# Performance work log

Measured on AMD Instinct MI355X. Metric: run time of the kernel, lower is better.

## Reference

```python
import jax, jax.numpy as jnp
import numpy as np

IN_DIMS = 32
HID = 64
N_HIDDEN = 5  # tcnn n_hidden_layers = hidden_layers + 1 = 5
OUT_DIMS = 3
BATCH = 2097152


def setup_inputs() -> dict:
    key = jax.random.key(0)
    ks = jax.random.split(key, N_HIDDEN + 2)
    x = jax.random.normal(ks[0], (BATCH, IN_DIMS), dtype=jnp.float32)
    # tcnn FullyFusedMLP has no biases; Kaiming-ish init scale
    W0 = jax.random.normal(ks[1], (IN_DIMS, HID), dtype=jnp.float32) * (1.0 / np.sqrt(IN_DIMS))
    Wh = jax.random.normal(ks[2], (N_HIDDEN - 1, HID, HID), dtype=jnp.float32) * (1.0 / np.sqrt(HID))
    Wo = jax.random.normal(ks[3], (HID, OUT_DIMS), dtype=jnp.float32) * (1.0 / np.sqrt(HID))
    return {"x": x, "W0": W0, "Wh": Wh, "Wo": Wo}


def reference(x, W0, Wh, Wo):
    # input layer -> ReLU
    h = jax.nn.relu(x @ W0)  # [B, 64]
    # 4 more hidden layers of 64->64 with ReLU (small fixed count, unrolled)
    for i in range(Wh.shape[0]):
        h = jax.nn.relu(h @ Wh[i])
    # linear output layer (output_activation = None)
    return h @ Wo  # [B, 3]
```

## Files before the change

kernel.cpp:

```cpp
#include <hip/hip_runtime.h>


typedef __attribute__((ext_vector_type(8))) short short8;
typedef __attribute__((ext_vector_type(4))) float f32x4;

#define BATCH   2097152
#define NBLOCKS 1024
#define NWAVES  (NBLOCKS * 4)
#define ITERS   (BATCH / (NWAVES * 16))
static_assert(BATCH == (size_t)NWAVES * 16 * ITERS, "");

__device__ __forceinline__ unsigned cvt_pk(float a, float b) {
    unsigned r;
    asm("v_cvt_pk_bf16_f32 %0, %1, %2" : "=v"(r) : "v"(a), "v"(b));
    return r;
}

__global__ __launch_bounds__(256, 4)
void mlp_fused(const float* __restrict__ x, const float* __restrict__ W0,
               const float* __restrict__ Wh, const float* __restrict__ Wo,
               float* __restrict__ out)
{
    __shared__ short8 wlds[38][64];

    const int tid  = threadIdx.x;
    const int w    = tid >> 6;
    const int lane = tid & 63;
    const int n = lane & 15;
    const int q = lane >> 4;

    const int gw = blockIdx.x * 4 + w;

    f32x4 raw0, raw1;
    {
        const f32x4* p = (const f32x4*)(x + ((size_t)gw * 16 + n) * 32) + 2 * q;
        raw0 = p[0]; raw1 = p[1];
    }

    int phi[4];
    #pragma unroll
    for (int t = 0; t < 4; ++t)
        phi[t] = 32 * (t >> 1) + 8 * (n >> 2) + 4 * (t & 1) + (n & 3);

    auto build = [&](const float* p) -> short8 {
        union { unsigned u[4]; short8 s; } f;
        #pragma unroll
        for (int i = 0; i < 4; ++i)
            f.u[i] = cvt_pk(p[(2 * i) * 64], p[(2 * i + 1) * 64]);
        return f.s;
    };
    if (w == 0) {
        #pragma unroll
        for (int t = 0; t < 4; ++t)
            wlds[t][lane] = build(W0 + (8 * q) * 64 + phi[t]);
        #pragma unroll
        for (int t = 0; t < 4; ++t)
            #pragma unroll
            for (int c = 0; c < 2; ++c)
                wlds[28 + 2 * t + c][lane] =
                    build(Wh + 3 * 4096 + (32 * c + 8 * q) * 64 + phi[t]);
        #pragma unroll
        for (int c = 0; c < 2; ++c) {
            union { unsigned u[4]; short8 s; } f;
            #pragma unroll
            for (int i = 0; i < 4; ++i) {
                float a = (n < 3) ? Wo[(32 * c + 8 * q + 2 * i)     * 3 + n] : 0.f;
                float b = (n < 3) ? Wo[(32 * c + 8 * q + 2 * i + 1) * 3 + n] : 0.f;
                f.u[i] = cvt_pk(a, b);
            }
            wlds[36 + c][lane] = f.s;
        }
    } else {
        const int l = w - 1;
        #pragma unroll
        for (int t = 0; t < 4; ++t)
            #pragma unroll
            for (int c = 0; c < 2; ++c)
                wlds[4 + 8 * l + 2 * t + c][lane] =
                    build(Wh + l * 4096 + (32 * c + 8 * q) * 64 + phi[t]);
    }
    __syncthreads();

    const f32x4 z = {0.f, 0.f, 0.f, 0.f};
    short8 X[8], Y[8];

    #pragma unroll
    for (int j = 0; j < 4; ++j) X[j] = wlds[j][lane];

    auto packact = [&](const f32x4 (&acc)[4], short8& b0, short8& b1) {
        union { unsigned u[4]; short8 s; } A, B;
        A.u[0] = cvt_pk(fmaxf(acc[0][0], 0.f), fmaxf(acc[0][1], 0.f));
        A.u[1] = cvt_pk(fmaxf(acc[0][2], 0.f), fmaxf(acc[0][3], 0.f));
        A.u[2] = cvt_pk(fmaxf(acc[1][0], 0.f), fmaxf(acc[1][1], 0.f));
        A.u[3] = cvt_pk(fmaxf(acc[1][2], 0.f), fmaxf(acc[1][3], 0.f));
        B.u[0] = cvt_pk(fmaxf(acc[2][0], 0.f), fmaxf(acc[2][1], 0.f));
        B.u[1] = cvt_pk(fmaxf(acc[2][2], 0.f), fmaxf(acc[2][3], 0.f));
        B.u[2] = cvt_pk(fmaxf(acc[3][0], 0.f), fmaxf(acc[3][1], 0.f));
        B.u[3] = cvt_pk(fmaxf(acc[3][2], 0.f), fmaxf(acc[3][3], 0.f));
        b0 = A.s; b1 = B.s;
    };

    #pragma unroll 1
    for (int it = 0; it < ITERS; ++it) {
        short8 xf;
        {
            union { unsigned u[4]; short8 s; } f;
            f.u[0] = cvt_pk(raw0[0], raw0[1]); f.u[1] = cvt_pk(raw0[2], raw0[3]);
            f.u[2] = cvt_pk(raw1[0], raw1[1]); f.u[3] = cvt_pk(raw1[2], raw1[3]);
            xf = f.s;
        }
        if (it + 1 < ITERS) {
            const size_t r = ((size_t)(it + 1) * NWAVES + gw) * 16;
            const f32x4* p = (const f32x4*)(x + (r + n) * 32) + 2 * q;
            raw0 = p[0]; raw1 = p[1];
        }
        const size_t row0 = ((size_t)it * NWAVES + gw) * 16;

        f32x4 acc[4];
        short8 b0, b1;

        #pragma unroll
        for (int j = 0; j < 8; ++j) Y[j] = wlds[4 + j][lane];
        #pragma unroll
        for (int t = 0; t < 4; ++t)
            acc[t] = __builtin_amdgcn_mfma_f32_16x16x32_bf16(X[t], xf, z, 0, 0, 0);

        #pragma unroll
        for (int j = 0; j < 8; ++j) X[j] = wlds[12 + j][lane];
        packact(acc, b0, b1);
        #pragma unroll
        for (int t = 0; t < 4; ++t)
            acc[t] = __builtin_amdgcn_mfma_f32_16x16x32_bf16(Y[2 * t], b0, z, 0, 0, 0);
        #pragma unroll
        for (int t = 0; t < 4; ++t)
            acc[t] = __builtin_amdgcn_mfma_f32_16x16x32_bf16(Y[2 * t + 1], b1, acc[t], 0, 0, 0);

        #pragma unroll
        for (int j = 0; j < 8; ++j) Y[j] = wlds[20 + j][lane];
        packact(acc, b0, b1);
        #pragma unroll
        for (int t = 0; t < 4; ++t)
            acc[t] = __builtin_amdgcn_mfma_f32_16x16x32_bf16(X[2 * t], b0, z, 0, 0, 0);
        #pragma unroll
        for (int t = 0; t < 4; ++t)
            acc[t] = __builtin_amdgcn_mfma_f32_16x16x32_bf16(X[2 * t + 1], b1, acc[t], 0, 0, 0);

        #pragma unroll
        for (int j = 0; j < 8; ++j) X[j] = wlds[28 + j][lane];
        packact(acc, b0, b1);
        #pragma unroll
        for (int t = 0; t < 4; ++t)
            acc[t] = __builtin_amdgcn_mfma_f32_16x16x32_bf16(Y[2 * t], b0, z, 0, 0, 0);
        #pragma unroll
        for (int t = 0; t < 4; ++t)
            acc[t] = __builtin_amdgcn_mfma_f32_16x16x32_bf16(Y[2 * t + 1], b1, acc[t], 0, 0, 0);

        Y[0] = wlds[36][lane];
        Y[1] = wlds[37][lane];
        packact(acc, b0, b1);
        #pragma unroll
        for (int t = 0; t < 4; ++t)
            acc[t] = __builtin_amdgcn_mfma_f32_16x16x32_bf16(X[2 * t], b0, z, 0, 0, 0);
        #pragma unroll
        for (int t = 0; t < 4; ++t)
            acc[t] = __builtin_amdgcn_mfma_f32_16x16x32_bf16(X[2 * t + 1], b1, acc[t], 0, 0, 0);

        #pragma unroll
        for (int j = 0; j < 4; ++j) X[j] = wlds[j][lane];
        packact(acc, b0, b1);
        f32x4 o = __builtin_amdgcn_mfma_f32_16x16x32_bf16(Y[0], b0, z, 0, 0, 0);
        o = __builtin_amdgcn_mfma_f32_16x16x32_bf16(Y[1], b1, o, 0, 0, 0);
        if (lane < 16) {
            float* po = out + (row0 + lane) * 3;
            po[0] = o[0]; po[1] = o[1]; po[2] = o[2];
        }
    }
}

extern "C" void kernel_launch(void* const* d_in, const int* in_sizes, int n_in,
                              void* d_out, int out_size, void* d_ws, size_t ws_size,
                              hipStream_t stream) {
    (void)in_sizes; (void)n_in; (void)d_ws; (void)ws_size; (void)out_size;
    const float* x  = (const float*)d_in[0];
    const float* W0 = (const float*)d_in[1];
    const float* Wh = (const float*)d_in[2];
    const float* Wo = (const float*)d_in[3];
    float* out = (float*)d_out;
    mlp_fused<<<NBLOCKS, 256, 0, stream>>>(x, W0, Wh, Wo, out);
}
```

Before: 377.4 us.

## Process four 16-row subtiles per wave iteration to amortize weight LDS loads

Each wave now handles 64 rows per loop iteration as four independent 16-row subtiles, so each layer's weight fragments read from LDS are reused across four MFMA chains. The four independent chains also give the scheduler more MFMA work to overlap dependency latency, and prefetching covers 64 rows of input. In exchange, register pressure rises (16 accumulators plus 8 raw input vectors), so launch bounds drop to 2 blocks per SIMD occupancy, and the loop runs fewer iterations.

```diff
diff --git a/kernel.cpp b/kernel.cpp
--- a/kernel.cpp
+++ b/kernel.cpp
@@ -7,8 +7,9 @@
 #define BATCH   2097152
 #define NBLOCKS 1024
 #define NWAVES  (NBLOCKS * 4)
-#define ITERS   (BATCH / (NWAVES * 16))
-static_assert(BATCH == (size_t)NWAVES * 16 * ITERS, "");
+#define ROWS_PW 64
+#define ITERS   (BATCH / (NWAVES * ROWS_PW))
+static_assert(BATCH == (size_t)NWAVES * ROWS_PW * ITERS, "");
 
 __device__ __forceinline__ unsigned cvt_pk(float a, float b) {
     unsigned r;
@@ -16,7 +17,7 @@
     return r;
 }
 
-__global__ __launch_bounds__(256, 4)
+__global__ __launch_bounds__(256, 2)
 void mlp_fused(const float* __restrict__ x, const float* __restrict__ W0,
                const float* __restrict__ Wh, const float* __restrict__ Wo,
                float* __restrict__ out)
@@ -31,10 +32,14 @@
 
     const int gw = blockIdx.x * 4 + w;
 
-    f32x4 raw0, raw1;
+    f32x4 raw[4][2];
     {
-        const f32x4* p = (const f32x4*)(x + ((size_t)gw * 16 + n) * 32) + 2 * q;
-        raw0 = p[0]; raw1 = p[1];
+        const size_t r = (size_t)gw * ROWS_PW;
+        #pragma unroll
+        for (int st = 0; st < 4; ++st) {
+            const f32x4* p = (const f32x4*)(x + (r + 16 * st + n) * 32) + 2 * q;
+            raw[st][0] = p[0]; raw[st][1] = p[1];
+        }
     }
 
     int phi[4];
@@ -102,77 +107,108 @@
 
     #pragma unroll 1
     for (int it = 0; it < ITERS; ++it) {
-        short8 xf;
-        {
+        const size_t row0 = ((size_t)it * NWAVES + gw) * ROWS_PW;
+        f32x4 acc[4][4];
+
+        #pragma unroll
+        for (int j = 0; j < 8; ++j) Y[j] = wlds[4 + j][lane];
+        #pragma unroll
+        for (int st = 0; st < 4; ++st) {
             union { unsigned u[4]; short8 s; } f;
-            f.u[0] = cvt_pk(raw0[0], raw0[1]); f.u[1] = cvt_pk(raw0[2], raw0[3]);
-            f.u[2] = cvt_pk(raw1[0], raw1[1]); f.u[3] = cvt_pk(raw1[2], raw1[3]);
-            xf = f.s;
+            f.u[0] = cvt_pk(raw[st][0][0], raw[st][0][1]);
+            f.u[1] = cvt_pk(raw[st][0][2], raw[st][0][3]);
+            f.u[2] = cvt_pk(raw[st][1][0], raw[st][1][1]);
+            f.u[3] = cvt_pk(raw[st][1][2], raw[st][1][3]);
+            #pragma unroll
+            for (int t = 0; t < 4; ++t)
+                acc[st][t] = __builtin_amdgcn_mfma_f32_16x16x32_bf16(
+                                 X[t], f.s, z, 0, 0, 0);
         }
         if (it + 1 < ITERS) {
-            const size_t r = ((size_t)(it + 1) * NWAVES + gw) * 16;
-            const f32x4* p = (const f32x4*)(x + (r + n) * 32) + 2 * q;
-            raw0 = p[0]; raw1 = p[1];
-        }
-        const size_t row0 = ((size_t)it * NWAVES + gw) * 16;
-
-        f32x4 acc[4];
-        short8 b0, b1;
-
-        #pragma unroll
-        for (int j = 0; j < 8; ++j) Y[j] = wlds[4 + j][lane];
-        #pragma unroll
-        for (int t = 0; t < 4; ++t)
-            acc[t] = __builtin_amdgcn_mfma_f32_16x16x32_bf16(X[t], xf, z, 0, 0, 0);
+            const size_t r = ((size_t)(it + 1) * NWAVES + gw) * ROWS_PW;
+            #pragma unroll
+            for (int st = 0; st < 4; ++st) {
+                const f32x4* p = (const f32x4*)(x + (r + 16 * st + n) * 32) + 2 * q;
+                raw[st][0] = p[0]; raw[st][1] = p[1];
+            }
+        }
 
         #pragma unroll
         for (int j = 0; j < 8; ++j) X[j] = wlds[12 + j][lane];
-        packact(acc, b0, b1);
-        #pragma unroll
-        for (int t = 0; t < 4; ++t)
-            acc[t] = __builtin_amdgcn_mfma_f32_16x16x32_bf16(Y[2 * t], b0, z, 0, 0, 0);
-        #pragma unroll
-        for (int t = 0; t < 4; ++t)
-            acc[t] = __builtin_amdgcn_mfma_f32_16x16x32_bf16(Y[2 * t + 1], b1, acc[t], 0, 0, 0);
+        #pragma unroll
+        for (int st = 0; st < 4; ++st) {
+            short8 b0, b1;
+            packact(acc[st], b0, b1);
+            #pragma unroll
+            for (int t = 0; t < 4; ++t)
+                acc[st][t] = __builtin_amdgcn_mfma_f32_16x16x32_bf16(
+                                 Y[2 * t], b0, z, 0, 0, 0);
+            #pragma unroll
+            for (int t = 0; t < 4; ++t)
+                acc[st][t] = __builtin_amdgcn_mfma_f32_16x16x32_bf16(
+                                 Y[2 * t + 1], b1, acc[st][t], 0, 0, 0);
+        }
 
         #pragma unroll
         for (int j = 0; j < 8; ++j) Y[j] = wlds[20 + j][lane];
-        packact(acc, b0, b1);
-        #pragma unroll
-        for (int t = 0; t < 4; ++t)
-            acc[t] = __builtin_amdgcn_mfma_f32_16x16x32_bf16(X[2 * t], b0, z, 0, 0, 0);
-        #pragma unroll
-        for (int t = 0; t < 4; ++t)
-            acc[t] = __builtin_amdgcn_mfma_f32_16x16x32_bf16(X[2 * t + 1], b1, acc[t], 0, 0, 0);
+        #pragma unroll
+        for (int st = 0; st < 4; ++st) {
+            short8 b0, b1;
+            packact(acc[st], b0, b1);
+            #pragma unroll
+            for (int t = 0; t < 4; ++t)
+                acc[st][t] = __builtin_amdgcn_mfma_f32_16x16x32_bf16(
+                                 X[2 * t], b0, z, 0, 0, 0);
+            #pragma unroll
+            for (int t = 0; t < 4; ++t)
+                acc[st][t] = __builtin_amdgcn_mfma_f32_16x16x32_bf16(
+                                 X[2 * t + 1], b1, acc[st][t], 0, 0, 0);
+        }
 
         #pragma unroll
         for (int j = 0; j < 8; ++j) X[j] = wlds[28 + j][lane];
-        packact(acc, b0, b1);
-        #pragma unroll
-        for (int t = 0; t < 4; ++t)
-            acc[t] = __builtin_amdgcn_mfma_f32_16x16x32_bf16(Y[2 * t], b0, z, 0, 0, 0);
-        #pragma unroll
-        for (int t = 0; t < 4; ++t)
-            acc[t] = __builtin_amdgcn_mfma_f32_16x16x32_bf16(Y[2 * t + 1], b1, acc[t], 0, 0, 0);
+        #pragma unroll
+        for (int st = 0; st < 4; ++st) {
+            short8 b0, b1;
+            packact(acc[st], b0, b1);
+            #pragma unroll
+            for (int t = 0; t < 4; ++t)
+                acc[st][t] = __builtin_amdgcn_mfma_f32_16x16x32_bf16(
+                                 Y[2 * t], b0, z, 0, 0, 0);
+            #pragma unroll
+            for (int t = 0; t < 4; ++t)
+                acc[st][t] = __builtin_amdgcn_mfma_f32_16x16x32_bf16(
+                                 Y[2 * t + 1], b1, acc[st][t], 0, 0, 0);
+        }
 
         Y[0] = wlds[36][lane];
         Y[1] = wlds[37][lane];
-        packact(acc, b0, b1);
-        #pragma unroll
-        for (int t = 0; t < 4; ++t)
-            acc[t] = __builtin_amdgcn_mfma_f32_16x16x32_bf16(X[2 * t], b0, z, 0, 0, 0);
-        #pragma unroll
-        for (int t = 0; t < 4; ++t)
-            acc[t] = __builtin_amdgcn_mfma_f32_16x16x32_bf16(X[2 * t + 1], b1, acc[t], 0, 0, 0);
+        #pragma unroll
+        for (int st = 0; st < 4; ++st) {
+            short8 b0, b1;
+            packact(acc[st], b0, b1);
+            #pragma unroll
+            for (int t = 0; t < 4; ++t)
+                acc[st][t] = __builtin_amdgcn_mfma_f32_16x16x32_bf16(
+                                 X[2 * t], b0, z, 0, 0, 0);
+            #pragma unroll
+            for (int t = 0; t < 4; ++t)
+                acc[st][t] = __builtin_amdgcn_mfma_f32_16x16x32_bf16(
+                                 X[2 * t + 1], b1, acc[st][t], 0, 0, 0);
+        }
 
         #pragma unroll
         for (int j = 0; j < 4; ++j) X[j] = wlds[j][lane];
-        packact(acc, b0, b1);
-        f32x4 o = __builtin_amdgcn_mfma_f32_16x16x32_bf16(Y[0], b0, z, 0, 0, 0);
-        o = __builtin_amdgcn_mfma_f32_16x16x32_bf16(Y[1], b1, o, 0, 0, 0);
-        if (lane < 16) {
-            float* po = out + (row0 + lane) * 3;
-            po[0] = o[0]; po[1] = o[1]; po[2] = o[2];
+        #pragma unroll
+        for (int st = 0; st < 4; ++st) {
+            short8 b0, b1;
+            packact(acc[st], b0, b1);
+            f32x4 o = __builtin_amdgcn_mfma_f32_16x16x32_bf16(Y[0], b0, z, 0, 0, 0);
+            o = __builtin_amdgcn_mfma_f32_16x16x32_bf16(Y[1], b1, o, 0, 0, 0);
+            if (lane < 16) {
+                float* po = out + (row0 + 16 * st + lane) * 3;
+                po[0] = o[0]; po[1] = o[1]; po[2] = o[2];
+            }
         }
     }
 }
```

New measurement: 386.8 us. 1.02x slower.
